# Kernel tuning notes

Hardware: AMD Instinct MI355X
Metric: run time of the kernel (lower is better)

## Reference

```python
import jax, jax.numpy as jnp
import numpy as np
from jax import lax

# dims
B, T = 64, 1024
ANNOT, RNN, MEM, ATTN = 512, 1024, 512, 512
FILTERS, KSIZE = 32, 31
PAD = (KSIZE - 1) // 2  # 15, SAME padding


def setup_inputs() -> dict:
    key = jax.random.key(0)
    ks = jax.random.split(key, 20)
    s = 0.02
    return {
        "memory": jax.random.normal(ks[0], (B, MEM), jnp.float32),
        "context": jax.random.normal(ks[1], (B, ANNOT), jnp.float32),
        "rnn_state": jax.random.normal(ks[2], (B, RNN), jnp.float32),
        "annots": jax.random.normal(ks[3], (B, T, ANNOT), jnp.float32),
        "atten": jax.random.uniform(ks[4], (B, 2, T), jnp.float32),
        "mask": jnp.ones((B, T), jnp.int32),
        "t": 0,
        # GRUCell params (torch gate order: r, z, n)
        "W_ih": jax.random.normal(ks[5], (3 * RNN, ANNOT + MEM), jnp.float32) * s,
        "W_hh": jax.random.normal(ks[6], (3 * RNN, RNN), jnp.float32) * s,
        "b_ih": jnp.zeros((3 * RNN,), jnp.float32),
        "b_hh": jnp.zeros((3 * RNN,), jnp.float32),
        # location-sensitive attention params
        "conv_w": jax.random.normal(ks[7], (FILTERS, 2, KSIZE), jnp.float32) * s,
        "loc_w": jax.random.normal(ks[8], (ATTN, FILTERS), jnp.float32) * s,
        "loc_b": jnp.zeros((ATTN,), jnp.float32),
        "q_w": jax.random.normal(ks[9], (ATTN, RNN), jnp.float32) * s,
        "q_b": jnp.zeros((ATTN,), jnp.float32),
        "a_w": jax.random.normal(ks[10], (ATTN, ANNOT), jnp.float32) * s,
        "a_b": jnp.zeros((ATTN,), jnp.float32),
        "v_w": jax.random.normal(ks[11], (1, ATTN), jnp.float32) * s,
    }


def _gru_cell(x, h, W_ih, W_hh, b_ih, b_hh):
    gi = x @ W_ih.T + b_ih  # [B, 3H]
    gh = h @ W_hh.T + b_hh
    i_r, i_z, i_n = jnp.split(gi, 3, axis=-1)
    h_r, h_z, h_n = jnp.split(gh, 3, axis=-1)
    r = jax.nn.sigmoid(i_r + h_r)
    z = jax.nn.sigmoid(i_z + h_z)
    n = jnp.tanh(i_n + r * h_n)
    return (1.0 - z) * n + z * h


def reference(memory, context, rnn_state, annots, atten, mask, t,
              W_ih, W_hh, b_ih, b_hh, conv_w, loc_w, loc_b,
              q_w, q_b, a_w, a_b, v_w):
    # GRU step on [memory; prev_context]
    rnn_input = jnp.concatenate([memory, context], axis=-1)  # [B, MEM+ANNOT]
    rnn_output = _gru_cell(rnn_input, rnn_state, W_ih, W_hh, b_ih, b_hh)  # [B, RNN]

    # location features: SAME conv over [B, 2, T] -> [B, FILTERS, T]
    loc_conv = lax.conv_general_dilated(
        atten, conv_w, window_strides=(1,), padding=[(PAD, PAD)],
        dimension_numbers=("NCH", "OIH", "NCH"))
    processed_loc = jnp.einsum("bft,af->bta", loc_conv, loc_w) + loc_b  # [B,T,ATTN]

    processed_query = (rnn_output @ q_w.T + q_b)[:, None, :]            # [B,1,ATTN]
    processed_annots = jnp.einsum("btd,ad->bta", annots, a_w) + a_b     # [B,T,ATTN]

    energy = jnp.tanh(processed_query + processed_annots + processed_loc)
    alignment = jnp.einsum("bta,a->bt", energy, v_w[0])                 # [B,T]

    # mask fill with -inf where mask == 0
    alignment = jnp.where(mask == 0, -jnp.inf, alignment)

    # sigmoid-normalized attention weights
    sig = jax.nn.sigmoid(alignment)
    alignment = sig / jnp.sum(sig, axis=1, keepdims=True)               # [B,T]

    new_context = jnp.einsum("bt,btd->bd", alignment, annots)           # [B,ANNOT]
    return rnn_output, new_context, alignment
```

## Files before the change

### kernel.cpp

```cpp
#include <hip/hip_runtime.h>

typedef float f32x4 __attribute__((ext_vector_type(4)));
typedef short bf16x8 __attribute__((ext_vector_type(8)));

__device__ __forceinline__ unsigned int pk2(float a, float b) {
    unsigned int ua = __float_as_uint(a); ua += 0x7FFFu + ((ua >> 16) & 1u);
    unsigned int ub = __float_as_uint(b); ub += 0x7FFFu + ((ub >> 16) & 1u);
    return __builtin_amdgcn_perm(ub, ua, 0x07060302u);
}
__device__ __forceinline__ unsigned short bf16_rne(float a) {
    unsigned int ua = __float_as_uint(a);
    ua += 0x7FFFu + ((ua >> 16) & 1u);
    return (unsigned short)(ua >> 16);
}
__device__ __forceinline__ float bf2f(unsigned int us) {
    return __uint_as_float(us << 16);
}
__device__ __forceinline__ float tanh_fast(float x) {
    float e = __expf(x + x);
    return 1.f - 2.f / (e + 1.f);
}
__device__ __forceinline__ f32x4 mfma16(bf16x8 a, bf16x8 b, f32x4 c) {
    return __builtin_amdgcn_mfma_f32_16x16x32_bf16(a, b, c, 0, 0, 0);
}
__device__ __forceinline__ void ald16(const void* g, void* l) {
    __builtin_amdgcn_global_load_lds(
        (const __attribute__((address_space(1))) unsigned int*)g,
        (__attribute__((address_space(3))) unsigned int*)l, 16, 0, 0);
}

#define NB_ANN  16384
#define Q_WIH   786432
#define Q_WHH   1572864
#define Q_QW    1703936
#define Q_X2    1720320
#define Q_X1    1736704
#define Q_BAW   1802240
#define Q_BLW   1806336
#define Q_EB    1806464
#define NB_CVT  7057
#define NB_PREP (NB_ANN + NB_CVT + 512)

__global__ __launch_bounds__(256) void k_prep(
    const float* __restrict__ annots, unsigned short* __restrict__ annb,
    const float* __restrict__ Wih, const float* __restrict__ Whh,
    const float* __restrict__ qw, const float* __restrict__ rnn_state,
    const float* __restrict__ memory, const float* __restrict__ context,
    const float* __restrict__ aw, const float* __restrict__ lw,
    const float* __restrict__ ab, const float* __restrict__ lb,
    const float* __restrict__ atten, const float* __restrict__ convw,
    unsigned short* __restrict__ Wihb, unsigned short* __restrict__ Whhb,
    unsigned short* __restrict__ qwb, unsigned short* __restrict__ X2b,
    unsigned short* __restrict__ X1b, unsigned short* __restrict__ Bbig,
    float* __restrict__ ebias, unsigned short* __restrict__ Lconv)
{
    __shared__ float att_s[2 * 160];
    __shared__ float cw_s[1984];
    const int tid = threadIdx.x;
    if (blockIdx.x < NB_ANN) {
        size_t i = ((size_t)blockIdx.x * 256 + tid) * 8;
        float4 v0 = *(const float4*)(annots + i);
        float4 v1 = *(const float4*)(annots + i + 4);
        uint4 u;
        u.x = pk2(v0.x, v0.y); u.y = pk2(v0.z, v0.w);
        u.z = pk2(v1.x, v1.y); u.w = pk2(v1.z, v1.w);
        *(uint4*)(annb + i) = u;
    } else if (blockIdx.x < NB_ANN + NB_CVT) {
        int q = (blockIdx.x - NB_ANN) * 256 + tid;
        if (q >= Q_EB) return;
        if (q < Q_WIH) {
            int i = q * 4;
            float4 v = *(const float4*)(Wih + i);
            uint2 u; u.x = pk2(v.x, v.y); u.y = pk2(v.z, v.w);
            *(uint2*)(Wihb + i) = u;
        } else if (q < Q_WHH) {
            int i = (q - Q_WIH) * 4;
            float4 v = *(const float4*)(Whh + i);
            uint2 u; u.x = pk2(v.x, v.y); u.y = pk2(v.z, v.w);
            *(uint2*)(Whhb + i) = u;
        } else if (q < Q_QW) {
            int i = (q - Q_WHH) * 4;
            float4 v = *(const float4*)(qw + i);
            uint2 u; u.x = pk2(v.x, v.y); u.y = pk2(v.z, v.w);
            *(uint2*)(qwb + i) = u;
        } else if (q < Q_X2) {
            int i = (q - Q_QW) * 4;
            float4 v = *(const float4*)(rnn_state + i);
            uint2 u; u.x = pk2(v.x, v.y); u.y = pk2(v.z, v.w);
            *(uint2*)(X2b + i) = u;
        } else if (q < Q_X1) {
            int i = (q - Q_X2) * 4;
            int b = i >> 10, c = i & 1023;
            const float* s = (c < 512) ? (memory + b * 512 + c) : (context + b * 512 + (c - 512));
            float4 v = *(const float4*)s;
            uint2 u; u.x = pk2(v.x, v.y); u.y = pk2(v.z, v.w);
            *(uint2*)(X1b + i) = u;
        } else if (q < Q_BAW) {
            int i = (q - Q_X1) * 4;
            int a = i >> 9, c = i & 511;
            float4 v = *(const float4*)(aw + a * 512 + c);
            uint2 u; u.x = pk2(v.x, v.y); u.y = pk2(v.z, v.w);
            *(uint2*)(Bbig + a * 544 + c) = u;
        } else if (q < Q_BLW) {
            int i = (q - Q_BAW) * 4;
            int a = i >> 5, c = i & 31;
            float4 v = *(const float4*)(lw + a * 32 + c);
            uint2 u; u.x = pk2(v.x, v.y); u.y = pk2(v.z, v.w);
            *(uint2*)(Bbig + a * 544 + 512 + c) = u;
        } else {
            int i = (q - Q_BLW) * 4;
            float4 va = *(const float4*)(ab + i);
            float4 vb = *(const float4*)(lb + i);
            float4 r; r.x = va.x + vb.x; r.y = va.y + vb.y; r.z = va.z + vb.z; r.w = va.w + vb.w;
            *(float4*)(ebias + i) = r;
        }
    } else {
        const int bid = blockIdx.x - (NB_ANN + NB_CVT);
        const int b = bid >> 3;
        const int tbase = (bid & 7) * 128;
        for (int i = tid; i < 320; i += 256) {
            int c = i / 160, j = i % 160;
            float v = 0.f;
            int pos = tbase - 15 + j;
            if (j < 158 && pos >= 0 && pos < 1024) v = atten[b * 2048 + c * 1024 + pos];
            att_s[c * 160 + j] = v;
        }
        for (int i = tid; i < 1984; i += 256) cw_s[i] = convw[i];
        __syncthreads();
        const int f = tid & 31, tq = tid >> 5;
        float acc[16];
#pragma unroll
        for (int i = 0; i < 16; ++i) acc[i] = 0.f;
        for (int c = 0; c < 2; ++c) {
            for (int k = 0; k < 31; ++k) {
                float w = cw_s[f * 62 + c * 31 + k];
                int base = c * 160 + tq * 16 + k;
#pragma unroll
                for (int ti = 0; ti < 16; ++ti) acc[ti] += w * att_s[base + ti];
            }
        }
#pragma unroll
        for (int ti = 0; ti < 16; ++ti) {
            int t = tbase + tq * 16 + ti;
            Lconv[(b * 1024 + t) * 32 + f] = bf16_rne(acc[ti]);
        }
    }
}

__global__ __launch_bounds__(256, 4) void k_gemm_ks(
    const unsigned short* __restrict__ A1, const unsigned short* __restrict__ A2,
    const unsigned short* __restrict__ B1, const unsigned short* __restrict__ B2,
    float* __restrict__ C, int N, int nTiles, int n_split, int K, int Klen)
{
    __shared__ __align__(16) unsigned short As[64 * 32];
    __shared__ __align__(16) unsigned short Bs[128 * 32];
    const int tid = threadIdx.x;
    const int nb = blockIdx.x % nTiles;
    const int ks = blockIdx.x / nTiles;
    const int nBase = nb * 128;
    const bool use2 = nBase >= n_split;
    const unsigned short* A = use2 ? A2 : A1;
    const unsigned short* B = use2 ? B2 : B1;
    const int brow0 = nBase - (use2 ? n_split : 0);
    const int lane = tid & 63, w = tid >> 6;
    const int c = lane & 15, qd = lane >> 4;
    const int lr = lane >> 2;
    const int swzl = ((lane & 3) ^ ((lr >> 1) & 3)) * 8;

    const f32x4 fz = {0.f, 0.f, 0.f, 0.f};
    f32x4 acc[4][2];
#pragma unroll
    for (int i = 0; i < 4; ++i) { acc[i][0] = fz; acc[i][1] = fz; }

    const int k0b = ks * Klen;
    const int nkc = Klen >> 5;
    for (int kc = 0; kc < nkc; ++kc) {
        const int k0 = k0b + kc * 32;
        ald16(A + (size_t)(w * 16 + lr) * K + k0 + swzl, &As[w * 512]);
        ald16(B + (size_t)(brow0 + w * 16 + lr) * K + k0 + swzl, &Bs[w * 512]);
        ald16(B + (size_t)(brow0 + 64 + w * 16 + lr) * K + k0 + swzl, &Bs[2048 + w * 512]);
        __syncthreads();
        const int rdoff = (qd ^ ((c >> 1) & 3)) * 8;
        bf16x8 af[4];
#pragma unroll
        for (int i = 0; i < 4; ++i) af[i] = *(const bf16x8*)&As[(i * 16 + c) * 32 + rdoff];
#pragma unroll
        for (int j = 0; j < 2; ++j) {
            bf16x8 bj = *(const bf16x8*)&Bs[(w * 32 + j * 16 + c) * 32 + rdoff];
#pragma unroll
            for (int i = 0; i < 4; ++i) acc[i][j] = mfma16(af[i], bj, acc[i][j]);
        }
        __syncthreads();
    }
    float* Cp = C + (size_t)ks * 64 * N;
#pragma unroll
    for (int i = 0; i < 4; ++i)
#pragma unroll
        for (int r = 0; r < 4; ++r) {
            int row = i * 16 + qd * 4 + r;
#pragma unroll
            for (int j = 0; j < 2; ++j) {
                int col = nBase + w * 32 + j * 16 + c;
                Cp[row * N + col] = acc[i][j][r];
            }
        }
}

__global__ __launch_bounds__(256) void k_gates(
    const float* __restrict__ Cg, const float* __restrict__ h0,
    const float* __restrict__ bih, const float* __restrict__ bhh,
    float* __restrict__ outv, unsigned short* __restrict__ X3b)
{
    int idx = blockIdx.x * 256 + threadIdx.x;
    int b = idx >> 10, h = idx & 1023;
    float s[6];
#pragma unroll
    for (int g = 0; g < 6; ++g) s[g] = 0.f;
#pragma unroll
    for (int ks = 0; ks < 4; ++ks) {
        const float* g = Cg + ks * 393216 + b * 6144 + h;
#pragma unroll
        for (int k = 0; k < 6; ++k) s[k] += g[k * 1024];
    }
    float ir = s[0] + bih[h], iz = s[1] + bih[h + 1024], inn = s[2] + bih[h + 2048];
    float hr = s[3] + bhh[h], hz = s[4] + bhh[h + 1024], hn = s[5] + bhh[h + 2048];
    float r = 1.f / (1.f + __expf(-(ir + hr)));
    float z = 1.f / (1.f + __expf(-(iz + hz)));
    float n = tanh_fast(inn + r * hn);
    float o = (1.f - z) * n + z * h0[idx];
    outv[idx] = o;
    X3b[idx] = bf16_rne(o);
}

__global__ __launch_bounds__(256, 4) void k_attn(
    const unsigned short* __restrict__ annb, const unsigned short* __restrict__ Lconv,
    const unsigned short* __restrict__ Bbig, const float* __restrict__ pqP,
    const float* __restrict__ qb, const float* __restrict__ ebias,
    const float* __restrict__ vw, float* __restrict__ wsal)
{
    __shared__ __align__(16) unsigned short As[64 * 32];
    __shared__ __align__(16) unsigned short Bs[256 * 32];
    __shared__ float red[4][64];
    const int tid = threadIdx.x;
    const int mtile = blockIdx.x >> 1;
    const int split = blockIdx.x & 1;
    const int btBase = mtile * 64;
    const int b = mtile >> 4;
    const int nb2 = split * 256;
    const int lane = tid & 63, w = tid >> 6;
    const int c = lane & 15, qd = lane >> 4;
    const int lr = lane >> 2;
    const int swzl = ((lane & 3) ^ ((lr >> 1) & 3)) * 8;

    const f32x4 fz = {0.f, 0.f, 0.f, 0.f};
    f32x4 acc[4][4];
#pragma unroll
    for (int i = 0; i < 4; ++i)
#pragma unroll
        for (int j = 0; j < 4; ++j) acc[i][j] = fz;

    const int arow = btBase + w * 16 + lr;
    for (int kc = 0; kc < 17; ++kc) {
        const int k0 = kc * 32;
        if (kc < 16)
            ald16(annb + (size_t)arow * 512 + k0 + swzl, &As[w * 512]);
        else
            ald16(Lconv + (size_t)arow * 32 + swzl, &As[w * 512]);
#pragma unroll
        for (int s = 0; s < 4; ++s)
            ald16(Bbig + (size_t)(nb2 + s * 64 + w * 16 + lr) * 544 + k0 + swzl,
                  &Bs[s * 2048 + w * 512]);
        __syncthreads();
        const int rdoff = (qd ^ ((c >> 1) & 3)) * 8;
        bf16x8 af[4];
#pragma unroll
        for (int i = 0; i < 4; ++i) af[i] = *(const bf16x8*)&As[(i * 16 + c) * 32 + rdoff];
#pragma unroll
        for (int j = 0; j < 4; ++j) {
            bf16x8 bj = *(const bf16x8*)&Bs[(w * 64 + j * 16 + c) * 32 + rdoff];
#pragma unroll
            for (int i = 0; i < 4; ++i) acc[i][j] = mfma16(af[i], bj, acc[i][j]);
        }
        __syncthreads();
    }
    float pe[4], vv[4];
#pragma unroll
    for (int j = 0; j < 4; ++j) {
        int colg = nb2 + w * 64 + j * 16 + c;
        float pq = qb[colg] + ebias[colg];
#pragma unroll
        for (int ks = 0; ks < 4; ++ks) pq += pqP[ks * 32768 + b * 512 + colg];
        pe[j] = pq;
        vv[j] = vw[colg];
    }
#pragma unroll
    for (int i = 0; i < 4; ++i)
#pragma unroll
        for (int r = 0; r < 4; ++r) {
            float p = 0.f;
#pragma unroll
            for (int j = 0; j < 4; ++j)
                p += vv[j] * tanh_fast(acc[i][j][r] + pe[j]);
            p += __shfl_xor(p, 1);
            p += __shfl_xor(p, 2);
            p += __shfl_xor(p, 4);
            p += __shfl_xor(p, 8);
            if (c == 0) red[w][i * 16 + qd * 4 + r] = p;
        }
    __syncthreads();
    if (tid < 64)
        wsal[split * 65536 + btBase + tid] = red[0][tid] + red[1][tid] + red[2][tid] + red[3][tid];
}

__global__ __launch_bounds__(256) void k_ctx(
    const unsigned short* __restrict__ annb, const float* __restrict__ wsal,
    const int* __restrict__ mask, float* __restrict__ out)
{
    __shared__ float al[1024];
    __shared__ float wsum[4];
    __shared__ float2 red[256];
    const int b = blockIdx.x >> 2;
    const int chunk = blockIdx.x & 3;
    const int tid = threadIdx.x;
    float lsum = 0.f;
#pragma unroll
    for (int p = 0; p < 4; ++p) {
        int t = p * 256 + tid;
        int bt = b * 1024 + t;
        float raw = wsal[bt] + wsal[65536 + bt];
        float s = (mask[bt] != 0) ? 1.f / (1.f + __expf(-raw)) : 0.f;
        al[t] = s;
        lsum += s;
    }
    for (int off = 32; off > 0; off >>= 1) lsum += __shfl_xor(lsum, off);
    if ((tid & 63) == 0) wsum[tid >> 6] = lsum;
    __syncthreads();
    const float tot = wsum[0] + wsum[1] + wsum[2] + wsum[3];
    const float inv = 1.f / tot;
    if (chunk == 0) {
#pragma unroll
        for (int p = 0; p < 4; ++p) {
            int t = p * 256 + tid;
            out[98304 + b * 1024 + t] = al[t] * inv;
        }
    }
    const int dq = tid & 63, tq = tid >> 6;
    const int d0 = chunk * 128 + dq * 2;
    const unsigned short* ap = annb + (size_t)(b * 1024 + tq * 256) * 512 + d0;
    float a0 = 0.f, a1 = 0.f;
#pragma unroll 4
    for (int t = 0; t < 256; ++t) {
        unsigned int u = *(const unsigned int*)(ap + (size_t)t * 512);
        float wgt = al[tq * 256 + t];
        a0 += wgt * bf2f(u & 0xFFFFu);
        a1 += wgt * bf2f(u >> 16);
    }
    red[tid].x = a0; red[tid].y = a1;
    __syncthreads();
    if (tid < 64) {
        float2 s2;
        s2.x = red[tid].x + red[64 + tid].x + red[128 + tid].x + red[192 + tid].x;
        s2.y = red[tid].y + red[64 + tid].y + red[128 + tid].y + red[192 + tid].y;
        float2 o; o.x = s2.x * inv; o.y = s2.y * inv;
        *(float2*)(out + 65536 + b * 512 + chunk * 128 + tid * 2) = o;
    }
}

extern "C" void kernel_launch(void* const* d_in, const int* in_sizes, int n_in,
                              void* d_out, int out_size, void* d_ws, size_t ws_size,
                              hipStream_t stream) {
    const float* memory    = (const float*)d_in[0];
    const float* context   = (const float*)d_in[1];
    const float* rnn_state = (const float*)d_in[2];
    const float* annots    = (const float*)d_in[3];
    const float* atten     = (const float*)d_in[4];
    const int*   mask      = (const int*)d_in[5];
    const float* W_ih   = (const float*)d_in[7];
    const float* W_hh   = (const float*)d_in[8];
    const float* b_ih   = (const float*)d_in[9];
    const float* b_hh   = (const float*)d_in[10];
    const float* conv_w = (const float*)d_in[11];
    const float* loc_w  = (const float*)d_in[12];
    const float* loc_b  = (const float*)d_in[13];
    const float* q_w    = (const float*)d_in[14];
    const float* q_b    = (const float*)d_in[15];
    const float* a_w    = (const float*)d_in[16];
    const float* a_b    = (const float*)d_in[17];
    const float* v_w    = (const float*)d_in[18];
    float* out = (float*)d_out;

    char* w8 = (char*)d_ws;
    unsigned short* Lconv = (unsigned short*)(w8 + 0);
    unsigned short* Bbig  = (unsigned short*)(w8 + 4194304);
    unsigned short* annb  = (unsigned short*)(w8 + 4751360);
    unsigned short* Wihb  = (unsigned short*)(w8 + 71860224);
    unsigned short* Whhb  = (unsigned short*)(w8 + 78151680);
    unsigned short* qwb   = (unsigned short*)(w8 + 84443136);
    unsigned short* X1b   = (unsigned short*)(w8 + 85491712);
    unsigned short* X2b   = (unsigned short*)(w8 + 85622784);
    unsigned short* X3b   = (unsigned short*)(w8 + 85753856);
    float*          Cgru  = (float*)(w8 + 85884928);
    float*          pqP   = (float*)(w8 + 92176384);
    float*          wsal  = (float*)(w8 + 92700672);
    float*          ebias = (float*)(w8 + 93224960);

    k_prep<<<NB_PREP, 256, 0, stream>>>(annots, annb,
                                        W_ih, W_hh, q_w, rnn_state, memory, context,
                                        a_w, loc_w, a_b, loc_b, atten, conv_w,
                                        Wihb, Whhb, qwb, X2b, X1b, Bbig, ebias, Lconv);
    k_gemm_ks<<<192, 256, 0, stream>>>(X1b, X2b, Wihb, Whhb, Cgru, 6144, 48, 3072, 1024, 256);
    k_gates<<<256, 256, 0, stream>>>(Cgru, rnn_state, b_ih, b_hh, out, X3b);
    k_gemm_ks<<<16, 256, 0, stream>>>(X3b, X3b, qwb, qwb, pqP, 512, 4, 0x40000000, 1024, 256);
    k_attn<<<2048, 256, 0, stream>>>(annb, Lconv, Bbig, pqP, q_b, ebias, v_w, wsal);
    k_ctx<<<256, 256, 0, stream>>>(annb, wsal, mask, out);
}
```

Measured before the change: 362.5 us.

## Drop bf16 annots copy, convert in-register, and bypass LDS in GEMMs

Removes the separate prep pass that converted the 128 MB fp32 annots tensor into a bf16 workspace copy. The attention GEMM now reads fp32 annots straight from global memory and converts them to bf16 in registers, with a register double-buffered prefetch. The GRU/query GEMMs and the attention kernel now load MFMA fragments directly from global memory instead of staging through LDS with barriers. The context kernel reads fp32 annots with a 1024-thread block layout. This saves a full write and reread of annots, but each attention block (two per row tile) now reads the fp32 data, doubling that traffic, and the direct fragment loads are less coalesced.

Measured after the change: 424.7 us. 1.17x slower.

```diff
diff --git a/kernel.cpp b/kernel.cpp
--- a/kernel.cpp
+++ b/kernel.cpp
@@ -13,9 +13,6 @@
     ua += 0x7FFFu + ((ua >> 16) & 1u);
     return (unsigned short)(ua >> 16);
 }
-__device__ __forceinline__ float bf2f(unsigned int us) {
-    return __uint_as_float(us << 16);
-}
 __device__ __forceinline__ float tanh_fast(float x) {
     float e = __expf(x + x);
     return 1.f - 2.f / (e + 1.f);
@@ -23,13 +20,16 @@
 __device__ __forceinline__ f32x4 mfma16(bf16x8 a, bf16x8 b, f32x4 c) {
     return __builtin_amdgcn_mfma_f32_16x16x32_bf16(a, b, c, 0, 0, 0);
 }
-__device__ __forceinline__ void ald16(const void* g, void* l) {
-    __builtin_amdgcn_global_load_lds(
-        (const __attribute__((address_space(1))) unsigned int*)g,
-        (__attribute__((address_space(3))) unsigned int*)l, 16, 0, 0);
-}
-
-#define NB_ANN  16384
+__device__ __forceinline__ bf16x8 as_bf(uint4 u) {
+    bf16x8 r; __builtin_memcpy(&r, &u, 16); return r;
+}
+__device__ __forceinline__ bf16x8 cvt_bf(float4 v0, float4 v1) {
+    uint4 u;
+    u.x = pk2(v0.x, v0.y); u.y = pk2(v0.z, v0.w);
+    u.z = pk2(v1.x, v1.y); u.w = pk2(v1.z, v1.w);
+    return as_bf(u);
+}
+
 #define Q_WIH   786432
 #define Q_WHH   1572864
 #define Q_QW    1703936
@@ -39,10 +39,8 @@
 #define Q_BLW   1806336
 #define Q_EB    1806464
 #define NB_CVT  7057
-#define NB_PREP (NB_ANN + NB_CVT + 512)
 
 __global__ __launch_bounds__(256) void k_prep(
-    const float* __restrict__ annots, unsigned short* __restrict__ annb,
     const float* __restrict__ Wih, const float* __restrict__ Whh,
     const float* __restrict__ qw, const float* __restrict__ rnn_state,
     const float* __restrict__ memory, const float* __restrict__ context,
@@ -57,16 +55,8 @@
     __shared__ float att_s[2 * 160];
     __shared__ float cw_s[1984];
     const int tid = threadIdx.x;
-    if (blockIdx.x < NB_ANN) {
-        size_t i = ((size_t)blockIdx.x * 256 + tid) * 8;
-        float4 v0 = *(const float4*)(annots + i);
-        float4 v1 = *(const float4*)(annots + i + 4);
-        uint4 u;
-        u.x = pk2(v0.x, v0.y); u.y = pk2(v0.z, v0.w);
-        u.z = pk2(v1.x, v1.y); u.w = pk2(v1.z, v1.w);
-        *(uint4*)(annb + i) = u;
-    } else if (blockIdx.x < NB_ANN + NB_CVT) {
-        int q = (blockIdx.x - NB_ANN) * 256 + tid;
+    if (blockIdx.x < NB_CVT) {
+        int q = blockIdx.x * 256 + tid;
         if (q >= Q_EB) return;
         if (q < Q_WIH) {
             int i = q * 4;
@@ -115,7 +105,7 @@
             *(float4*)(ebias + i) = r;
         }
     } else {
-        const int bid = blockIdx.x - (NB_ANN + NB_CVT);
+        const int bid = blockIdx.x - NB_CVT;
         const int b = bid >> 3;
         const int tbase = (bid & 7) * 128;
         for (int i = tid; i < 320; i += 256) {
@@ -147,13 +137,11 @@
     }
 }
 
-__global__ __launch_bounds__(256, 4) void k_gemm_ks(
+__global__ __launch_bounds__(256, 4) void k_gemm_nolds(
     const unsigned short* __restrict__ A1, const unsigned short* __restrict__ A2,
     const unsigned short* __restrict__ B1, const unsigned short* __restrict__ B2,
     float* __restrict__ C, int N, int nTiles, int n_split, int K, int Klen)
 {
-    __shared__ __align__(16) unsigned short As[64 * 32];
-    __shared__ __align__(16) unsigned short Bs[128 * 32];
     const int tid = threadIdx.x;
     const int nb = blockIdx.x % nTiles;
     const int ks = blockIdx.x / nTiles;
@@ -164,8 +152,13 @@
     const int brow0 = nBase - (use2 ? n_split : 0);
     const int lane = tid & 63, w = tid >> 6;
     const int c = lane & 15, qd = lane >> 4;
-    const int lr = lane >> 2;
-    const int swzl = ((lane & 3) ^ ((lr >> 1) & 3)) * 8;
+
+    const unsigned short* ap[4];
+    const unsigned short* bp[2];
+#pragma unroll
+    for (int i = 0; i < 4; ++i) ap[i] = A + (size_t)(i * 16 + c) * K + qd * 8;
+#pragma unroll
+    for (int j = 0; j < 2; ++j) bp[j] = B + (size_t)(brow0 + w * 32 + j * 16 + c) * K + qd * 8;
 
     const f32x4 fz = {0.f, 0.f, 0.f, 0.f};
     f32x4 acc[4][2];
@@ -174,23 +167,18 @@
 
     const int k0b = ks * Klen;
     const int nkc = Klen >> 5;
+#pragma unroll 2
     for (int kc = 0; kc < nkc; ++kc) {
         const int k0 = k0b + kc * 32;
-        ald16(A + (size_t)(w * 16 + lr) * K + k0 + swzl, &As[w * 512]);
-        ald16(B + (size_t)(brow0 + w * 16 + lr) * K + k0 + swzl, &Bs[w * 512]);
-        ald16(B + (size_t)(brow0 + 64 + w * 16 + lr) * K + k0 + swzl, &Bs[2048 + w * 512]);
-        __syncthreads();
-        const int rdoff = (qd ^ ((c >> 1) & 3)) * 8;
-        bf16x8 af[4];
-#pragma unroll
-        for (int i = 0; i < 4; ++i) af[i] = *(const bf16x8*)&As[(i * 16 + c) * 32 + rdoff];
-#pragma unroll
-        for (int j = 0; j < 2; ++j) {
-            bf16x8 bj = *(const bf16x8*)&Bs[(w * 32 + j * 16 + c) * 32 + rdoff];
-#pragma unroll
-            for (int i = 0; i < 4; ++i) acc[i][j] = mfma16(af[i], bj, acc[i][j]);
-        }
-        __syncthreads();
+        bf16x8 af[4], bf[2];
+#pragma unroll
+        for (int i = 0; i < 4; ++i) af[i] = *(const bf16x8*)(ap[i] + k0);
+#pragma unroll
+        for (int j = 0; j < 2; ++j) bf[j] = *(const bf16x8*)(bp[j] + k0);
+#pragma unroll
+        for (int j = 0; j < 2; ++j)
+#pragma unroll
+            for (int i = 0; i < 4; ++i) acc[i][j] = mfma16(af[i], bf[j], acc[i][j]);
     }
     float* Cp = C + (size_t)ks * 64 * N;
 #pragma unroll
@@ -232,14 +220,12 @@
     X3b[idx] = bf16_rne(o);
 }
 
-__global__ __launch_bounds__(256, 4) void k_attn(
-    const unsigned short* __restrict__ annb, const unsigned short* __restrict__ Lconv,
+__global__ __launch_bounds__(256, 2) void k_attn(
+    const float* __restrict__ annots, const unsigned short* __restrict__ Lconv,
     const unsigned short* __restrict__ Bbig, const float* __restrict__ pqP,
     const float* __restrict__ qb, const float* __restrict__ ebias,
     const float* __restrict__ vw, float* __restrict__ wsal)
 {
-    __shared__ __align__(16) unsigned short As[64 * 32];
-    __shared__ __align__(16) unsigned short Bs[256 * 32];
     __shared__ float red[4][64];
     const int tid = threadIdx.x;
     const int mtile = blockIdx.x >> 1;
@@ -249,8 +235,16 @@
     const int nb2 = split * 256;
     const int lane = tid & 63, w = tid >> 6;
     const int c = lane & 15, qd = lane >> 4;
-    const int lr = lane >> 2;
-    const int swzl = ((lane & 3) ^ ((lr >> 1) & 3)) * 8;
+
+    const float* ap[4];
+    const unsigned short* bp[4];
+    const unsigned short* lp[4];
+#pragma unroll
+    for (int i = 0; i < 4; ++i) {
+        ap[i] = annots + (size_t)(btBase + i * 16 + c) * 512 + qd * 8;
+        lp[i] = Lconv + (size_t)(btBase + i * 16 + c) * 32 + qd * 8;
+        bp[i] = Bbig + (size_t)(nb2 + w * 64 + i * 16 + c) * 544 + qd * 8;
+    }
 
     const f32x4 fz = {0.f, 0.f, 0.f, 0.f};
     f32x4 acc[4][4];
@@ -259,30 +253,57 @@
 #pragma unroll
         for (int j = 0; j < 4; ++j) acc[i][j] = fz;
 
-    const int arow = btBase + w * 16 + lr;
-    for (int kc = 0; kc < 17; ++kc) {
-        const int k0 = kc * 32;
-        if (kc < 16)
-            ald16(annb + (size_t)arow * 512 + k0 + swzl, &As[w * 512]);
-        else
-            ald16(Lconv + (size_t)arow * 32 + swzl, &As[w * 512]);
-#pragma unroll
-        for (int s = 0; s < 4; ++s)
-            ald16(Bbig + (size_t)(nb2 + s * 64 + w * 16 + lr) * 544 + k0 + swzl,
-                  &Bs[s * 2048 + w * 512]);
-        __syncthreads();
-        const int rdoff = (qd ^ ((c >> 1) & 3)) * 8;
-        bf16x8 af[4];
-#pragma unroll
-        for (int i = 0; i < 4; ++i) af[i] = *(const bf16x8*)&As[(i * 16 + c) * 32 + rdoff];
-#pragma unroll
-        for (int j = 0; j < 4; ++j) {
-            bf16x8 bj = *(const bf16x8*)&Bs[(w * 64 + j * 16 + c) * 32 + rdoff];
-#pragma unroll
-            for (int i = 0; i < 4; ++i) acc[i][j] = mfma16(af[i], bj, acc[i][j]);
-        }
-        __syncthreads();
-    }
+    float4 ra0[4], ra1[4];
+    uint4 rb[4];
+#pragma unroll
+    for (int i = 0; i < 4; ++i) {
+        ra0[i] = *(const float4*)(ap[i]);
+        ra1[i] = *(const float4*)(ap[i] + 4);
+        rb[i] = *(const uint4*)(bp[i]);
+    }
+    uint4 rta[4];
+
+#pragma unroll 5
+    for (int kc = 0; kc < 15; ++kc) {
+        bf16x8 af[4], bf[4];
+#pragma unroll
+        for (int i = 0; i < 4; ++i) { af[i] = cvt_bf(ra0[i], ra1[i]); bf[i] = as_bf(rb[i]); }
+        const int k0 = (kc + 1) * 32;
+#pragma unroll
+        for (int i = 0; i < 4; ++i) {
+            ra0[i] = *(const float4*)(ap[i] + k0);
+            ra1[i] = *(const float4*)(ap[i] + k0 + 4);
+            rb[i] = *(const uint4*)(bp[i] + k0);
+        }
+#pragma unroll
+        for (int j = 0; j < 4; ++j)
+#pragma unroll
+            for (int i = 0; i < 4; ++i) acc[i][j] = mfma16(af[i], bf[j], acc[i][j]);
+    }
+    {
+        bf16x8 af[4], bf[4];
+#pragma unroll
+        for (int i = 0; i < 4; ++i) { af[i] = cvt_bf(ra0[i], ra1[i]); bf[i] = as_bf(rb[i]); }
+#pragma unroll
+        for (int i = 0; i < 4; ++i) {
+            rta[i] = *(const uint4*)(lp[i]);
+            rb[i] = *(const uint4*)(bp[i] + 512);
+        }
+#pragma unroll
+        for (int j = 0; j < 4; ++j)
+#pragma unroll
+            for (int i = 0; i < 4; ++i) acc[i][j] = mfma16(af[i], bf[j], acc[i][j]);
+    }
+    {
+        bf16x8 af[4], bf[4];
+#pragma unroll
+        for (int i = 0; i < 4; ++i) { af[i] = as_bf(rta[i]); bf[i] = as_bf(rb[i]); }
+#pragma unroll
+        for (int j = 0; j < 4; ++j)
+#pragma unroll
+            for (int i = 0; i < 4; ++i) acc[i][j] = mfma16(af[i], bf[j], acc[i][j]);
+    }
+
     float pe[4], vv[4];
 #pragma unroll
     for (int j = 0; j < 4; ++j) {
@@ -312,57 +333,42 @@
         wsal[split * 65536 + btBase + tid] = red[0][tid] + red[1][tid] + red[2][tid] + red[3][tid];
 }
 
-__global__ __launch_bounds__(256) void k_ctx(
-    const unsigned short* __restrict__ annb, const float* __restrict__ wsal,
+__global__ __launch_bounds__(1024) void k_ctx(
+    const float* __restrict__ annots, const float* __restrict__ wsal,
     const int* __restrict__ mask, float* __restrict__ out)
 {
     __shared__ float al[1024];
-    __shared__ float wsum[4];
-    __shared__ float2 red[256];
-    const int b = blockIdx.x >> 2;
-    const int chunk = blockIdx.x & 3;
+    __shared__ float wsum[16];
+    __shared__ float red[16][64];
+    const int b = blockIdx.x >> 3;
+    const int chunk = blockIdx.x & 7;
     const int tid = threadIdx.x;
-    float lsum = 0.f;
-#pragma unroll
-    for (int p = 0; p < 4; ++p) {
-        int t = p * 256 + tid;
-        int bt = b * 1024 + t;
-        float raw = wsal[bt] + wsal[65536 + bt];
-        float s = (mask[bt] != 0) ? 1.f / (1.f + __expf(-raw)) : 0.f;
-        al[t] = s;
-        lsum += s;
-    }
-    for (int off = 32; off > 0; off >>= 1) lsum += __shfl_xor(lsum, off);
-    if ((tid & 63) == 0) wsum[tid >> 6] = lsum;
+    const int bt = b * 1024 + tid;
+    float raw = wsal[bt] + wsal[65536 + bt];
+    float s = (mask[bt] != 0) ? 1.f / (1.f + __expf(-raw)) : 0.f;
+    al[tid] = s;
+    float ls = s;
+    for (int off = 32; off > 0; off >>= 1) ls += __shfl_xor(ls, off);
+    if ((tid & 63) == 0) wsum[tid >> 6] = ls;
     __syncthreads();
-    const float tot = wsum[0] + wsum[1] + wsum[2] + wsum[3];
+    float tot = 0.f;
+#pragma unroll
+    for (int i = 0; i < 16; ++i) tot += wsum[i];
     const float inv = 1.f / tot;
-    if (chunk == 0) {
-#pragma unroll
-        for (int p = 0; p < 4; ++p) {
-            int t = p * 256 + tid;
-            out[98304 + b * 1024 + t] = al[t] * inv;
-        }
-    }
+    if (chunk == 0) out[98304 + bt] = s * inv;
+
     const int dq = tid & 63, tq = tid >> 6;
-    const int d0 = chunk * 128 + dq * 2;
-    const unsigned short* ap = annb + (size_t)(b * 1024 + tq * 256) * 512 + d0;
-    float a0 = 0.f, a1 = 0.f;
-#pragma unroll 4
-    for (int t = 0; t < 256; ++t) {
-        unsigned int u = *(const unsigned int*)(ap + (size_t)t * 512);
-        float wgt = al[tq * 256 + t];
-        a0 += wgt * bf2f(u & 0xFFFFu);
-        a1 += wgt * bf2f(u >> 16);
-    }
-    red[tid].x = a0; red[tid].y = a1;
+    const float* ap = annots + (size_t)(b * 1024 + tq * 64) * 512 + chunk * 64 + dq;
+    float acc = 0.f;
+#pragma unroll 8
+    for (int t = 0; t < 64; ++t) acc += al[tq * 64 + t] * ap[(size_t)t * 512];
+    red[tq][dq] = acc;
     __syncthreads();
     if (tid < 64) {
-        float2 s2;
-        s2.x = red[tid].x + red[64 + tid].x + red[128 + tid].x + red[192 + tid].x;
-        s2.y = red[tid].y + red[64 + tid].y + red[128 + tid].y + red[192 + tid].y;
-        float2 o; o.x = s2.x * inv; o.y = s2.y * inv;
-        *(float2*)(out + 65536 + b * 512 + chunk * 128 + tid * 2) = o;
+        float s2 = 0.f;
+#pragma unroll
+        for (int i = 0; i < 16; ++i) s2 += red[i][tid];
+        out[65536 + b * 512 + chunk * 64 + tid] = s2 * inv;
     }
 }
 
@@ -392,25 +398,23 @@
     char* w8 = (char*)d_ws;
     unsigned short* Lconv = (unsigned short*)(w8 + 0);
     unsigned short* Bbig  = (unsigned short*)(w8 + 4194304);
-    unsigned short* annb  = (unsigned short*)(w8 + 4751360);
-    unsigned short* Wihb  = (unsigned short*)(w8 + 71860224);
-    unsigned short* Whhb  = (unsigned short*)(w8 + 78151680);
-    unsigned short* qwb   = (unsigned short*)(w8 + 84443136);
-    unsigned short* X1b   = (unsigned short*)(w8 + 85491712);
-    unsigned short* X2b   = (unsigned short*)(w8 + 85622784);
-    unsigned short* X3b   = (unsigned short*)(w8 + 85753856);
-    float*          Cgru  = (float*)(w8 + 85884928);
-    float*          pqP   = (float*)(w8 + 92176384);
-    float*          wsal  = (float*)(w8 + 92700672);
-    float*          ebias = (float*)(w8 + 93224960);
-
-    k_prep<<<NB_PREP, 256, 0, stream>>>(annots, annb,
-                                        W_ih, W_hh, q_w, rnn_state, memory, context,
-                                        a_w, loc_w, a_b, loc_b, atten, conv_w,
-                                        Wihb, Whhb, qwb, X2b, X1b, Bbig, ebias, Lconv);
-    k_gemm_ks<<<192, 256, 0, stream>>>(X1b, X2b, Wihb, Whhb, Cgru, 6144, 48, 3072, 1024, 256);
+    unsigned short* Wihb  = (unsigned short*)(w8 + 4751360);
+    unsigned short* Whhb  = (unsigned short*)(w8 + 11042816);
+    unsigned short* qwb   = (unsigned short*)(w8 + 17334272);
+    unsigned short* X1b   = (unsigned short*)(w8 + 18382848);
+    unsigned short* X2b   = (unsigned short*)(w8 + 18513920);
+    unsigned short* X3b   = (unsigned short*)(w8 + 18644992);
+    float*          Cgru  = (float*)(w8 + 18776064);
+    float*          pqP   = (float*)(w8 + 25067520);
+    float*          wsal  = (float*)(w8 + 25591808);
+    float*          ebias = (float*)(w8 + 26116096);
+
+    k_prep<<<NB_CVT + 512, 256, 0, stream>>>(W_ih, W_hh, q_w, rnn_state, memory, context,
+                                             a_w, loc_w, a_b, loc_b, atten, conv_w,
+                                             Wihb, Whhb, qwb, X2b, X1b, Bbig, ebias, Lconv);
+    k_gemm_nolds<<<192, 256, 0, stream>>>(X1b, X2b, Wihb, Whhb, Cgru, 6144, 48, 3072, 1024, 256);
     k_gates<<<256, 256, 0, stream>>>(Cgru, rnn_state, b_ih, b_hh, out, X3b);
-    k_gemm_ks<<<16, 256, 0, stream>>>(X3b, X3b, qwb, qwb, pqP, 512, 4, 0x40000000, 1024, 256);
-    k_attn<<<2048, 256, 0, stream>>>(annb, Lconv, Bbig, pqP, q_b, ebias, v_w, wsal);
-    k_ctx<<<256, 256, 0, stream>>>(annb, wsal, mask, out);
-}
+    k_gemm_nolds<<<16, 256, 0, stream>>>(X3b, X3b, qwb, qwb, pqP, 512, 4, 0x40000000, 1024, 256);
+    k_attn<<<2048, 256, 0, stream>>>(annots, Lconv, Bbig, pqP, q_b, ebias, v_w, wsal);
+    k_ctx<<<512, 1024, 0, stream>>>(annots, wsal, mask, out);
+}
```
